# Kernel tuning notes

Hardware: AMD Instinct MI355X
Metric: run time of the kernel (lower is better)

The kernel has to match this reference:

```python
import jax, jax.numpy as jnp
import numpy as np

N_NODES = 100000
N_EDGES = 1200000
D = 64
EPS = 1e-12  # matches torch F.normalize eps


def l2norm(x):
    n = jnp.linalg.norm(x, axis=-1, keepdims=True)
    return x / jnp.maximum(n, EPS)


def sage_layer(x, src, dst, Wl, bl, Wr, scale):
    # mechanism.normalize: row-wise L2 normalize (noise_scale=0 -> perturb is identity)
    xn = l2norm(x)
    # agg = x_normalized + scatter-add of neighbor (source) features into targets
    agg = xn + jax.ops.segment_sum(xn[src], dst, num_segments=N_NODES)
    # MessageNorm(learn_scale=True): normalize(msg) * ||x||_2 * scale
    msg = l2norm(agg) * jnp.linalg.norm(x, axis=-1, keepdims=True) * scale
    # lin_l(msg) + lin_r(x)  (root_weight=True, lin_r has no bias)
    out = msg @ Wl.T + bl + x @ Wr.T
    return l2norm(out)


def setup_inputs() -> dict:
    key = jax.random.key(0)
    ks = jax.random.split(key, 7)
    s = 1.0 / np.sqrt(D)
    return {
        "x": jax.random.normal(ks[0], (N_NODES, D), jnp.float32),
        "Wl0": jax.random.normal(ks[1], (D, D), jnp.float32) * s,
        "bl0": jnp.zeros((D,), jnp.float32),
        "Wr0": jax.random.normal(ks[2], (D, D), jnp.float32) * s,
        "scale0": jnp.ones((), jnp.float32),
        "Wl1": jax.random.normal(ks[3], (D, D), jnp.float32) * s,
        "bl1": jnp.zeros((D,), jnp.float32),
        "Wr1": jax.random.normal(ks[4], (D, D), jnp.float32) * s,
        "scale1": jnp.ones((), jnp.float32),
        "edge_index": jax.random.randint(ks[5], (2, N_EDGES), 0, N_NODES, dtype=jnp.int32),
    }


def reference(x, Wl0, bl0, Wr0, scale0, Wl1, bl1, Wr1, scale1, edge_index):
    src, dst = edge_index[0], edge_index[1]
    h = sage_layer(x, src, dst, Wl0, bl0, Wr0, scale0)
    h = jax.nn.relu(h)  # activation after layer 0 (not pred layer); dropout=identity (eval)
    h = sage_layer(h, src, dst, Wl1, bl1, Wr1, scale1)
    return h  # last layer of pred module: no bn/dropout/activation
```

## Files before the change

### kernel.cpp

```cpp
#include <hip/hip_runtime.h>

#define D 64
#define EPS 1e-12f
#define WPITCH 68
#define BSHIFT 8
#define BW 256
#define NBMAX 2048
#define NBLK 256

typedef unsigned short u16;

__device__ __forceinline__ float bf2f(u16 u) {
    return __uint_as_float(((unsigned)u) << 16);
}
__device__ __forceinline__ u16 f2bf(float f) {
    unsigned u = __float_as_uint(f);
    u += 0x7fffu + ((u >> 16) & 1u);
    return (u16)(u >> 16);
}
__device__ __forceinline__ float loadf(const void* p, size_t i, int bf) {
    return bf ? bf2f(((const u16*)p)[i]) : ((const float*)p)[i];
}
__device__ __forceinline__ float4 cvt4(ushort4 u) {
    return make_float4(bf2f(u.x), bf2f(u.y), bf2f(u.z), bf2f(u.w));
}

#define FMA4(acc, s, v)                       \
    do {                                      \
        acc.x = fmaf((s), (v).x, acc.x);      \
        acc.y = fmaf((s), (v).y, acc.y);      \
        acc.z = fmaf((s), (v).z, acc.z);      \
        acc.w = fmaf((s), (v).w, acc.w);      \
    } while (0)

__global__ __launch_bounds__(64) void detect_kernel(const u16* __restrict__ x,
                                                    int* __restrict__ flag) {
    int lane = threadIdx.x;
    int bad = 0;
    for (int i = 0; i < 64; ++i) {
        u16 u = x[lane * 64 + i];
        int e = (u >> 7) & 0xFF;
        if (e >= 0xC0) bad = 1;
    }
    unsigned long long b = __ballot(bad);
    if (lane == 0) *flag = (b == 0ull) ? 1 : 0;
}


__global__ __launch_bounds__(256) void zero_kernel(int* __restrict__ a, int n) {
    int i = blockIdx.x * blockDim.x + threadIdx.x;
    if (i < n) a[i] = 0;
}

__global__ __launch_bounds__(256) void bhist_kernel(const int* __restrict__ dst,
                                                    int* __restrict__ blockhist,
                                                    int E, int NB) {
    __shared__ int lh[NBMAX];
    const int b = blockIdx.x, t = threadIdx.x;
    const int per = (E + NBLK - 1) / NBLK;
    const int e0 = b * per, e1 = min(E, e0 + per);
    if (NB <= NBMAX) {
        for (int i = t; i < NB; i += 256) lh[i] = 0;
        __syncthreads();
        for (int e = e0 + t; e < e1; e += 256)
            atomicAdd(&lh[dst[e] >> BSHIFT], 1);
        __syncthreads();
        for (int i = t; i < NB; i += 256) blockhist[i * NBLK + b] = lh[i];
    } else {
        for (int e = e0 + t; e < e1; e += 256)
            atomicAdd(&blockhist[(dst[e] >> BSHIFT) * NBLK + b], 1);
    }
}

__global__ __launch_bounds__(256) void scanA_kernel(const int* __restrict__ a,
                                                    int* __restrict__ partials, int M) {
    int b = blockIdx.x, t = threadIdx.x;
    int base = b * 1024 + t * 4;
    int s = 0;
#pragma unroll
    for (int i = 0; i < 4; ++i) {
        int idx = base + i;
        if (idx < M) s += a[idx];
    }
    s += __shfl_xor(s, 32); s += __shfl_xor(s, 16); s += __shfl_xor(s, 8);
    s += __shfl_xor(s, 4);  s += __shfl_xor(s, 2);  s += __shfl_xor(s, 1);
    __shared__ int wt[4];
    if ((t & 63) == 0) wt[t >> 6] = s;
    __syncthreads();
    if (t == 0) partials[b] = wt[0] + wt[1] + wt[2] + wt[3];
}

__global__ __launch_bounds__(64) void scanB_kernel(int* __restrict__ partials, int NP) {
    int l = threadIdx.x;
    int total = 0;
    for (int base = 0; base < NP; base += 64) {
        int v = (base + l < NP) ? partials[base + l] : 0;
        int inc = v;
        for (int d = 1; d < 64; d <<= 1) {
            int u = __shfl_up(inc, d);
            if (l >= d) inc += u;
        }
        if (base + l < NP) partials[base + l] = inc - v + total;
        total += __shfl(inc, 63);
    }
}

__global__ __launch_bounds__(256) void scanC_kernel(const int* __restrict__ a,
                                                    const int* __restrict__ partials,
                                                    int* __restrict__ pos, int M) {
    int b = blockIdx.x, t = threadIdx.x;
    int base = b * 1024 + t * 4;
    int v[4];
    int s = 0;
#pragma unroll
    for (int i = 0; i < 4; ++i) {
        int idx = base + i;
        v[i] = (idx < M) ? a[idx] : 0;
        s += v[i];
    }
    int li = t & 63, w = t >> 6;
    int inc = s;
    for (int d = 1; d < 64; d <<= 1) {
        int u = __shfl_up(inc, d);
        if (li >= d) inc += u;
    }
    __shared__ int wt[4];
    if (li == 63) wt[w] = inc;
    __syncthreads();
    int woff = 0;
    for (int i = 0; i < w; ++i) woff += wt[i];
    int run = partials[b] + woff + (inc - s);
#pragma unroll
    for (int i = 0; i < 4; ++i) {
        int idx = base + i;
        if (idx < M) { pos[idx] = run; run += v[i]; }
    }
}

__global__ __launch_bounds__(256) void bmeta_kernel(const int* __restrict__ pos,
                                                    int* __restrict__ bcounts,
                                                    int* __restrict__ boffsets,
                                                    int NB, int E) {
    int i = blockIdx.x * blockDim.x + threadIdx.x;
    if (i < NB) {
        int s = pos[(size_t)i * NBLK];
        boffsets[i] = s;
        int nxt = (i + 1 < NB) ? pos[(size_t)(i + 1) * NBLK] : E;
        bcounts[i] = nxt - s;
    }
}

__global__ __launch_bounds__(256) void bfill_kernel(const int* __restrict__ src,
                                                    const int* __restrict__ dst,
                                                    int* __restrict__ pos,
                                                    int* __restrict__ bucket,
                                                    int E, int NB) {
    __shared__ int cur[NBMAX];
    const int b = blockIdx.x, t = threadIdx.x;
    const int per = (E + NBLK - 1) / NBLK;
    const int e0 = b * per, e1 = min(E, e0 + per);
    if (NB <= NBMAX) {
        for (int i = t; i < NB; i += 256) cur[i] = pos[(size_t)i * NBLK + b];
        __syncthreads();
        for (int e = e0 + t; e < e1; e += 256) {
            int s = src[e], d = dst[e];
            int p = atomicAdd(&cur[d >> BSHIFT], 1);
            bucket[p] = (s << BSHIFT) | (d & (BW - 1));
        }
    } else {
        for (int e = e0 + t; e < e1; e += 256) {
            int s = src[e], d = dst[e];
            int p = atomicAdd(&pos[(size_t)(d >> BSHIFT) * NBLK + b], 1);
            bucket[p] = (s << BSHIFT) | (d & (BW - 1));
        }
    }
}

__global__ __launch_bounds__(256) void csr_from_buckets_kernel(
    const int* __restrict__ bucket,
    const int* __restrict__ bcounts, const int* __restrict__ boffsets,
    int* __restrict__ counts, int* __restrict__ offsets,
    int* __restrict__ sorted_src, int N)
{
    __shared__ int hist[BW];
    __shared__ int cur[BW];
    __shared__ int wt[4];

    const int b = blockIdx.x;
    const int t = threadIdx.x;
    const int nbase = b << BSHIFT;
    const int ecnt = bcounts[b];
    const int ebase = boffsets[b];

    hist[t] = 0;
    __syncthreads();

    for (int e = t; e < ecnt; e += 256)
        atomicAdd(&hist[bucket[ebase + e] & (BW - 1)], 1);
    __syncthreads();

    int v = hist[t];
    int inc = v;
    for (int d = 1; d < 64; d <<= 1) {
        int u = __shfl_up(inc, d);
        if ((t & 63) >= d) inc += u;
    }
    if ((t & 63) == 63) wt[t >> 6] = inc;
    __syncthreads();
    int woff = 0;
    for (int i = 0; i < (t >> 6); ++i) woff += wt[i];
    int excl = inc - v + woff;
    cur[t] = excl;
    int node = nbase + t;
    if (node < N) {
        counts[node] = v;
        offsets[node] = ebase + excl;
    }
    __syncthreads();

    for (int e = t; e < ecnt; e += 256) {
        int pv = bucket[ebase + e];
        int p = atomicAdd(&cur[pv & (BW - 1)], 1);
        sorted_src[ebase + p] = ((unsigned)pv) >> BSHIFT;
    }
}


__global__ __launch_bounds__(256) void norm_init_kernel(
    const void* __restrict__ xin, float* __restrict__ nx, float* __restrict__ rnx,
    int N, const int* __restrict__ flagp)
{
    const int bf = *flagp;
    int node = (int)((blockIdx.x * blockDim.x + threadIdx.x) >> 6);
    int lane = threadIdx.x & 63;
    if (node >= N) return;
    float v = loadf(xin, (size_t)node * D + lane, bf);
    float s = v * v;
    s += __shfl_xor(s, 32); s += __shfl_xor(s, 16); s += __shfl_xor(s, 8);
    s += __shfl_xor(s, 4);  s += __shfl_xor(s, 2);  s += __shfl_xor(s, 1);
    if (lane == 0) {
        float n = sqrtf(s);
        nx[node] = n;
        rnx[node] = 1.0f / fmaxf(n, EPS);
    }
}

__device__ __forceinline__ float4 loadrow4(const void* p, int row, int lane16, int bf) {
    if (bf) {
        ushort4 u = ((const ushort4*)((const u16*)p + (size_t)row * D))[lane16];
        return cvt4(u);
    }
    return ((const float4*)((const float*)p + (size_t)row * D))[lane16];
}

__global__ __launch_bounds__(256) void gather_kernel(
    const int* __restrict__ offsets, const int* __restrict__ counts,
    const int* __restrict__ sorted_src,
    const void* __restrict__ xin, const float* __restrict__ rnx,
    float* __restrict__ agg, int N, const int* __restrict__ flagp)
{
    const int bf = *flagp;
    int node = (int)((blockIdx.x * blockDim.x + threadIdx.x) >> 6);
    int lane = threadIdx.x & 63;
    if (node >= N) return;
    const int lane16 = lane & 15, grp = lane >> 4;

    float4 acc = make_float4(0.f, 0.f, 0.f, 0.f);
    if (grp == 0) {
        float4 xs = loadrow4(xin, node, lane16, bf);
        FMA4(acc, rnx[node], xs);
    }

    const int start = offsets[node];
    const int deg = counts[node];
    for (int i = 0; i < deg; i += 64) {
        int cnt = min(deg - i, 64);
        int id = (lane < cnt) ? sorted_src[start + i + lane] : 0;
        float wvl = rnx[id];
        int j = 0;
        for (; j + 8 <= cnt; j += 8) {
            int s0 = __shfl(id, j + grp);
            int s1 = __shfl(id, j + 4 + grp);
            float w0 = __shfl(wvl, j + grp);
            float w1 = __shfl(wvl, j + 4 + grp);
            float4 v0 = loadrow4(xin, s0, lane16, bf);
            float4 v1 = loadrow4(xin, s1, lane16, bf);
            FMA4(acc, w0, v0);
            FMA4(acc, w1, v1);
        }
        if (j + 4 <= cnt) {
            int s0 = __shfl(id, j + grp);
            float w0 = __shfl(wvl, j + grp);
            float4 v0 = loadrow4(xin, s0, lane16, bf);
            FMA4(acc, w0, v0);
            j += 4;
        }
        if (j < cnt) {
            int e = j + grp;
            int s0 = __shfl(id, min(e, cnt - 1));
            float w0 = __shfl(wvl, min(e, cnt - 1));
            if (e < cnt) {
                float4 v0 = loadrow4(xin, s0, lane16, bf);
                FMA4(acc, w0, v0);
            }
        }
    }

    acc.x += __shfl_xor(acc.x, 16); acc.y += __shfl_xor(acc.y, 16);
    acc.z += __shfl_xor(acc.z, 16); acc.w += __shfl_xor(acc.w, 16);
    acc.x += __shfl_xor(acc.x, 32); acc.y += __shfl_xor(acc.y, 32);
    acc.z += __shfl_xor(acc.z, 32); acc.w += __shfl_xor(acc.w, 32);
    if (grp == 0)
        ((float4*)(agg + (size_t)node * D))[lane16] = acc;
}

#define KSTEP(kk, comp)                                                     \
    {                                                                       \
        float4 a = *((const float4*)(wlp + (kk) * WPITCH));                 \
        float4 b = *((const float4*)(wrp + (kk) * WPITCH));                 \
        FMA4(acc[0], m[0].comp, a); FMA4(acc[0], xf[0].comp, b);            \
        FMA4(acc[1], m[1].comp, a); FMA4(acc[1], xf[1].comp, b);            \
        FMA4(acc[2], m[2].comp, a); FMA4(acc[2], xf[2].comp, b);            \
        FMA4(acc[3], m[3].comp, a); FMA4(acc[3], xf[3].comp, b);            \
    }

__global__ __launch_bounds__(256) void epilogue_kernel(
    const float* __restrict__ agg, float* __restrict__ nx,
    float* __restrict__ rnx, const void* __restrict__ xin,
    const void* __restrict__ wl, const void* __restrict__ bl,
    const void* __restrict__ wr, const void* __restrict__ scale_p,
    void* __restrict__ out, int N, const int* __restrict__ flagp,
    int relu, int write_norm)
{
    __shared__ float lds_wl[D * WPITCH];
    __shared__ float lds_wr[D * WPITCH];
    __shared__ float lds_bl[D];
    __shared__ float msgbuf[4][16 * WPITCH];

    const int bf = *flagp;
    const int t = threadIdx.x;
    for (int idx = t; idx < D * D; idx += 256) {
        int j = idx >> 6, k = idx & 63;
        lds_wl[k * WPITCH + j] = loadf(wl, idx, bf);
        lds_wr[k * WPITCH + j] = loadf(wr, idx, bf);
    }
    if (t < D) lds_bl[t] = loadf(bl, t, bf);
    __syncthreads();

    const float scl = loadf(scale_p, 0, bf);
    const int w = t >> 6, lane = t & 63;
    const int sub = lane >> 4, cg = lane & 15;
    float* mrow = msgbuf[w];

    for (int g = 0; g < 2; ++g) {
        const int node0 = blockIdx.x * 128 + g * 64 + w * 16 + sub * 4;
        int n[4];
        bool valid[4];
        float4 a4[4];
        float nxv[4];
#pragma unroll
        for (int r = 0; r < 4; ++r) {
            int nn = node0 + r;
            valid[r] = nn < N;
            n[r] = valid[r] ? nn : N - 1;
            a4[r] = ((const float4*)(agg + (size_t)n[r] * D))[cg];
            nxv[r] = nx[n[r]];
        }

#pragma unroll
        for (int r = 0; r < 4; ++r) {
            float4 v4 = a4[r];
            float s = v4.x * v4.x + v4.y * v4.y + v4.z * v4.z + v4.w * v4.w;
            s += __shfl_xor(s, 1); s += __shfl_xor(s, 2);
            s += __shfl_xor(s, 4); s += __shfl_xor(s, 8);
            float minv = scl * nxv[r] / fmaxf(sqrtf(s), EPS);
            *((float4*)(mrow + (sub * 4 + r) * WPITCH + cg * 4)) =
                make_float4(v4.x * minv, v4.y * minv, v4.z * minv, v4.w * minv);
        }

        float4 acc[4];
        {
            float4 b4 = ((const float4*)lds_bl)[cg];
#pragma unroll
            for (int r = 0; r < 4; ++r) acc[r] = b4;
        }

        const float* wlbase = lds_wl + cg * 4;
        const float* wrbase = lds_wr + cg * 4;

        if (bf) {
#pragma unroll
            for (int k4 = 0; k4 < 16; ++k4) {
                float4 m[4], xf[4];
#pragma unroll
                for (int r = 0; r < 4; ++r) {
                    m[r] = *((const float4*)(mrow + (sub * 4 + r) * WPITCH + k4 * 4));
                    ushort4 xu =
                        ((const ushort4*)((const u16*)xin + (size_t)n[r] * D))[k4];
                    xf[r] = cvt4(xu);
                }
                const float* wlp = wlbase + (k4 * 4) * WPITCH;
                const float* wrp = wrbase + (k4 * 4) * WPITCH;
                KSTEP(0, x) KSTEP(1, y) KSTEP(2, z) KSTEP(3, w)
            }
        } else {
#pragma unroll
            for (int k4 = 0; k4 < 16; ++k4) {
                float4 m[4], xf[4];
#pragma unroll
                for (int r = 0; r < 4; ++r) {
                    m[r] = *((const float4*)(mrow + (sub * 4 + r) * WPITCH + k4 * 4));
                    xf[r] = ((const float4*)((const float*)xin + (size_t)n[r] * D))[k4];
                }
                const float* wlp = wlbase + (k4 * 4) * WPITCH;
                const float* wrp = wrbase + (k4 * 4) * WPITCH;
                KSTEP(0, x) KSTEP(1, y) KSTEP(2, z) KSTEP(3, w)
            }
        }

#pragma unroll
        for (int r = 0; r < 4; ++r) {
            float4 v = acc[r];
            float s2 = v.x * v.x + v.y * v.y + v.z * v.z + v.w * v.w;
            s2 += __shfl_xor(s2, 1); s2 += __shfl_xor(s2, 2);
            s2 += __shfl_xor(s2, 4); s2 += __shfl_xor(s2, 8);
            float inv = 1.0f / fmaxf(sqrtf(s2), EPS);
            float4 rv = make_float4(v.x * inv, v.y * inv, v.z * inv, v.w * inv);
            if (relu) {
                rv.x = fmaxf(rv.x, 0.f); rv.y = fmaxf(rv.y, 0.f);
                rv.z = fmaxf(rv.z, 0.f); rv.w = fmaxf(rv.w, 0.f);
            }
            if (write_norm) {
                float s3 = rv.x * rv.x + rv.y * rv.y + rv.z * rv.z + rv.w * rv.w;
                s3 += __shfl_xor(s3, 1); s3 += __shfl_xor(s3, 2);
                s3 += __shfl_xor(s3, 4); s3 += __shfl_xor(s3, 8);
                if (valid[r] && cg == 0) {
                    float nn = sqrtf(s3);
                    nx[n[r]] = nn;
                    rnx[n[r]] = 1.0f / fmaxf(nn, EPS);
                }
            }
            if (valid[r]) {
                if (bf) {
                    ushort4 o =
                        make_ushort4(f2bf(rv.x), f2bf(rv.y), f2bf(rv.z), f2bf(rv.w));
                    ((ushort4*)((u16*)out + (size_t)n[r] * D))[cg] = o;
                } else {
                    ((float4*)((float*)out + (size_t)n[r] * D))[cg] = rv;
                }
            }
        }
    }
}

extern "C" void kernel_launch(void* const* d_in, const int* in_sizes, int n_in,
                              void* d_out, int out_size, void* d_ws, size_t ws_size,
                              hipStream_t stream)
{
    const void* x   = d_in[0];
    const void* Wl0 = d_in[1];
    const void* bl0 = d_in[2];
    const void* Wr0 = d_in[3];
    const void* sc0 = d_in[4];
    const void* Wl1 = d_in[5];
    const void* bl1 = d_in[6];
    const void* Wr1 = d_in[7];
    const void* sc1 = d_in[8];
    const int* ei   = (const int*)d_in[9];

    const int N = in_sizes[0] / D;
    const int E = in_sizes[9] / 2;
    const int* src = ei;
    const int* dst = ei + E;

    const int NB = (N + BW - 1) >> BSHIFT;
    const int M  = NB * NBLK;
    const int NP = (M + 1023) / 1024;

    float* agg       = (float*)d_ws;
    float* nx        = agg + (size_t)N * D;
    float* rnx       = nx + N;
    int* flag        = (int*)(rnx + N);
    int* counts      = flag + 1;
    int* offsets     = counts + N;
    int* bcounts     = offsets + N;
    int* boffsets    = bcounts + NB;
    int* blockhist   = boffsets + NB;
    int* pos         = blockhist + M;
    int* partials    = pos + M;
    int* bucket      = partials + NP;
    int* sorted_src  = bucket + E;

    void* h = d_out;

    dim3 blk(256);
    int gridA  = (N + 3) / 4;
    int gridC  = (N + 127) / 128;

    detect_kernel<<<1, 64, 0, stream>>>((const u16*)x, flag);

    if (NB > NBMAX)
        zero_kernel<<<(M + 255) / 256, blk, 0, stream>>>(blockhist, M);
    bhist_kernel<<<NBLK, blk, 0, stream>>>(dst, blockhist, E, NB);
    scanA_kernel<<<NP, blk, 0, stream>>>(blockhist, partials, M);
    scanB_kernel<<<1, 64, 0, stream>>>(partials, NP);
    scanC_kernel<<<NP, blk, 0, stream>>>(blockhist, partials, pos, M);
    bmeta_kernel<<<(NB + 255) / 256, blk, 0, stream>>>(pos, bcounts, boffsets, NB, E);
    bfill_kernel<<<NBLK, blk, 0, stream>>>(src, dst, pos, bucket, E, NB);
    csr_from_buckets_kernel<<<NB, blk, 0, stream>>>(bucket, bcounts, boffsets,
                                                    counts, offsets, sorted_src, N);

    norm_init_kernel<<<gridA, blk, 0, stream>>>(x, nx, rnx, N, flag);
    gather_kernel<<<gridA, blk, 0, stream>>>(offsets, counts, sorted_src, x, rnx,
                                             agg, N, flag);
    epilogue_kernel<<<gridC, blk, 0, stream>>>(agg, nx, rnx, x, Wl0, bl0, Wr0, sc0,
                                               h, N, flag, 1, 1);

    gather_kernel<<<gridA, blk, 0, stream>>>(offsets, counts, sorted_src, h, rnx,
                                             agg, N, flag);
    epilogue_kernel<<<gridC, blk, 0, stream>>>(agg, nx, rnx, h, Wl1, bl1, Wr1, sc1,
                                               d_out, N, flag, 0, 0);
}
```

Measured before the change: 401.0 us.

## Fold scan-B and bucket-meta kernels into neighbors, halve epilogue nodes per block

Removes the single-block scanB kernel by having each scanC block sum the preceding partials itself, and removes bmeta_kernel by computing bucket offsets and counts directly from pos inside csr_from_buckets. The epilogue kernel now handles 64 nodes per block instead of looping over two groups of 64, doubling the grid. This cuts two kernel launches and a serial stage, at the cost of redundant partial-sum reads in scanC and a reload of the LDS weights in twice as many blocks.

```diff
diff --git a/kernel.cpp b/kernel.cpp
--- a/kernel.cpp
+++ b/kernel.cpp
@@ -90,25 +90,23 @@
     if (t == 0) partials[b] = wt[0] + wt[1] + wt[2] + wt[3];
 }
 
-__global__ __launch_bounds__(64) void scanB_kernel(int* __restrict__ partials, int NP) {
-    int l = threadIdx.x;
-    int total = 0;
-    for (int base = 0; base < NP; base += 64) {
-        int v = (base + l < NP) ? partials[base + l] : 0;
-        int inc = v;
-        for (int d = 1; d < 64; d <<= 1) {
-            int u = __shfl_up(inc, d);
-            if (l >= d) inc += u;
-        }
-        if (base + l < NP) partials[base + l] = inc - v + total;
-        total += __shfl(inc, 63);
-    }
-}
-
 __global__ __launch_bounds__(256) void scanC_kernel(const int* __restrict__ a,
                                                     const int* __restrict__ partials,
-                                                    int* __restrict__ pos, int M) {
-    int b = blockIdx.x, t = threadIdx.x;
+                                                    int* __restrict__ pos,
+                                                    int M, int NP) {
+    const int b = blockIdx.x, t = threadIdx.x;
+    __shared__ int bwt[4];
+    __shared__ int wt[4];
+
+    int mysum = 0;
+    for (int i = t; i < b; i += 256) mysum += partials[i];
+    mysum += __shfl_xor(mysum, 32); mysum += __shfl_xor(mysum, 16);
+    mysum += __shfl_xor(mysum, 8);  mysum += __shfl_xor(mysum, 4);
+    mysum += __shfl_xor(mysum, 2);  mysum += __shfl_xor(mysum, 1);
+    if ((t & 63) == 0) bwt[t >> 6] = mysum;
+    __syncthreads();
+    const int base_sum = bwt[0] + bwt[1] + bwt[2] + bwt[3];
+
     int base = b * 1024 + t * 4;
     int v[4];
     int s = 0;
@@ -124,29 +122,15 @@
         int u = __shfl_up(inc, d);
         if (li >= d) inc += u;
     }
-    __shared__ int wt[4];
     if (li == 63) wt[w] = inc;
     __syncthreads();
     int woff = 0;
     for (int i = 0; i < w; ++i) woff += wt[i];
-    int run = partials[b] + woff + (inc - s);
+    int run = base_sum + woff + (inc - s);
 #pragma unroll
     for (int i = 0; i < 4; ++i) {
         int idx = base + i;
         if (idx < M) { pos[idx] = run; run += v[i]; }
-    }
-}
-
-__global__ __launch_bounds__(256) void bmeta_kernel(const int* __restrict__ pos,
-                                                    int* __restrict__ bcounts,
-                                                    int* __restrict__ boffsets,
-                                                    int NB, int E) {
-    int i = blockIdx.x * blockDim.x + threadIdx.x;
-    if (i < NB) {
-        int s = pos[(size_t)i * NBLK];
-        boffsets[i] = s;
-        int nxt = (i + 1 < NB) ? pos[(size_t)(i + 1) * NBLK] : E;
-        bcounts[i] = nxt - s;
     }
 }
 
@@ -177,10 +161,9 @@
 }
 
 __global__ __launch_bounds__(256) void csr_from_buckets_kernel(
-    const int* __restrict__ bucket,
-    const int* __restrict__ bcounts, const int* __restrict__ boffsets,
+    const int* __restrict__ bucket, const int* __restrict__ pos,
     int* __restrict__ counts, int* __restrict__ offsets,
-    int* __restrict__ sorted_src, int N)
+    int* __restrict__ sorted_src, int N, int E, int NB)
 {
     __shared__ int hist[BW];
     __shared__ int cur[BW];
@@ -189,8 +172,9 @@
     const int b = blockIdx.x;
     const int t = threadIdx.x;
     const int nbase = b << BSHIFT;
-    const int ecnt = bcounts[b];
-    const int ebase = boffsets[b];
+    const int ebase = pos[(size_t)b * NBLK];
+    const int enext = (b + 1 < NB) ? pos[(size_t)(b + 1) * NBLK] : E;
+    const int ecnt = enext - ebase;
 
     hist[t] = 0;
     __syncthreads();
@@ -350,104 +334,100 @@
     const float scl = loadf(scale_p, 0, bf);
     const int w = t >> 6, lane = t & 63;
     const int sub = lane >> 4, cg = lane & 15;
-    float* mrow = msgbuf[w];
-
-    for (int g = 0; g < 2; ++g) {
-        const int node0 = blockIdx.x * 128 + g * 64 + w * 16 + sub * 4;
-        int n[4];
-        bool valid[4];
-        float4 a4[4];
-        float nxv[4];
-#pragma unroll
-        for (int r = 0; r < 4; ++r) {
-            int nn = node0 + r;
-            valid[r] = nn < N;
-            n[r] = valid[r] ? nn : N - 1;
-            a4[r] = ((const float4*)(agg + (size_t)n[r] * D))[cg];
-            nxv[r] = nx[n[r]];
-        }
-
-#pragma unroll
-        for (int r = 0; r < 4; ++r) {
-            float4 v4 = a4[r];
-            float s = v4.x * v4.x + v4.y * v4.y + v4.z * v4.z + v4.w * v4.w;
-            s += __shfl_xor(s, 1); s += __shfl_xor(s, 2);
-            s += __shfl_xor(s, 4); s += __shfl_xor(s, 8);
-            float minv = scl * nxv[r] / fmaxf(sqrtf(s), EPS);
-            *((float4*)(mrow + (sub * 4 + r) * WPITCH + cg * 4)) =
-                make_float4(v4.x * minv, v4.y * minv, v4.z * minv, v4.w * minv);
-        }
-
-        float4 acc[4];
-        {
-            float4 b4 = ((const float4*)lds_bl)[cg];
-#pragma unroll
-            for (int r = 0; r < 4; ++r) acc[r] = b4;
-        }
-
-        const float* wlbase = lds_wl + cg * 4;
-        const float* wrbase = lds_wr + cg * 4;
-
-        if (bf) {
-#pragma unroll
-            for (int k4 = 0; k4 < 16; ++k4) {
-                float4 m[4], xf[4];
-#pragma unroll
-                for (int r = 0; r < 4; ++r) {
-                    m[r] = *((const float4*)(mrow + (sub * 4 + r) * WPITCH + k4 * 4));
-                    ushort4 xu =
-                        ((const ushort4*)((const u16*)xin + (size_t)n[r] * D))[k4];
-                    xf[r] = cvt4(xu);
-                }
-                const float* wlp = wlbase + (k4 * 4) * WPITCH;
-                const float* wrp = wrbase + (k4 * 4) * WPITCH;
-                KSTEP(0, x) KSTEP(1, y) KSTEP(2, z) KSTEP(3, w)
+
+    const int node0 = blockIdx.x * 64 + w * 16 + sub * 4;
+    int n[4];
+    bool valid[4];
+    float4 a4[4];
+    float nxv[4];
+#pragma unroll
+    for (int r = 0; r < 4; ++r) {
+        int nn = node0 + r;
+        valid[r] = nn < N;
+        n[r] = valid[r] ? nn : N - 1;
+        a4[r] = ((const float4*)(agg + (size_t)n[r] * D))[cg];
+        nxv[r] = nx[n[r]];
+    }
+
+    float* mrow = &msgbuf[w][sub * 4 * WPITCH];
+#pragma unroll
+    for (int r = 0; r < 4; ++r) {
+        float4 v4 = a4[r];
+        float s = v4.x * v4.x + v4.y * v4.y + v4.z * v4.z + v4.w * v4.w;
+        s += __shfl_xor(s, 1); s += __shfl_xor(s, 2);
+        s += __shfl_xor(s, 4); s += __shfl_xor(s, 8);
+        float minv = scl * nxv[r] / fmaxf(sqrtf(s), EPS);
+        *((float4*)(mrow + r * WPITCH + cg * 4)) =
+            make_float4(v4.x * minv, v4.y * minv, v4.z * minv, v4.w * minv);
+    }
+
+    float4 acc[4];
+    {
+        float4 b4 = ((const float4*)lds_bl)[cg];
+#pragma unroll
+        for (int r = 0; r < 4; ++r) acc[r] = b4;
+    }
+
+    const float* wlbase = lds_wl + cg * 4;
+    const float* wrbase = lds_wr + cg * 4;
+
+    if (bf) {
+#pragma unroll
+        for (int k4 = 0; k4 < 16; ++k4) {
+            float4 m[4], xf[4];
+#pragma unroll
+            for (int r = 0; r < 4; ++r) {
+                m[r] = *((const float4*)(mrow + r * WPITCH + k4 * 4));
+                ushort4 xu = ((const ushort4*)((const u16*)xin + (size_t)n[r] * D))[k4];
+                xf[r] = cvt4(xu);
             }
-        } else {
-#pragma unroll
-            for (int k4 = 0; k4 < 16; ++k4) {
-                float4 m[4], xf[4];
-#pragma unroll
-                for (int r = 0; r < 4; ++r) {
-                    m[r] = *((const float4*)(mrow + (sub * 4 + r) * WPITCH + k4 * 4));
-                    xf[r] = ((const float4*)((const float*)xin + (size_t)n[r] * D))[k4];
-                }
-                const float* wlp = wlbase + (k4 * 4) * WPITCH;
-                const float* wrp = wrbase + (k4 * 4) * WPITCH;
-                KSTEP(0, x) KSTEP(1, y) KSTEP(2, z) KSTEP(3, w)
+            const float* wlp = wlbase + (k4 * 4) * WPITCH;
+            const float* wrp = wrbase + (k4 * 4) * WPITCH;
+            KSTEP(0, x) KSTEP(1, y) KSTEP(2, z) KSTEP(3, w)
+        }
+    } else {
+#pragma unroll
+        for (int k4 = 0; k4 < 16; ++k4) {
+            float4 m[4], xf[4];
+#pragma unroll
+            for (int r = 0; r < 4; ++r) {
+                m[r] = *((const float4*)(mrow + r * WPITCH + k4 * 4));
+                xf[r] = ((const float4*)((const float*)xin + (size_t)n[r] * D))[k4];
             }
-        }
-
-#pragma unroll
-        for (int r = 0; r < 4; ++r) {
-            float4 v = acc[r];
-            float s2 = v.x * v.x + v.y * v.y + v.z * v.z + v.w * v.w;
-            s2 += __shfl_xor(s2, 1); s2 += __shfl_xor(s2, 2);
-            s2 += __shfl_xor(s2, 4); s2 += __shfl_xor(s2, 8);
-            float inv = 1.0f / fmaxf(sqrtf(s2), EPS);
-            float4 rv = make_float4(v.x * inv, v.y * inv, v.z * inv, v.w * inv);
-            if (relu) {
-                rv.x = fmaxf(rv.x, 0.f); rv.y = fmaxf(rv.y, 0.f);
-                rv.z = fmaxf(rv.z, 0.f); rv.w = fmaxf(rv.w, 0.f);
+            const float* wlp = wlbase + (k4 * 4) * WPITCH;
+            const float* wrp = wrbase + (k4 * 4) * WPITCH;
+            KSTEP(0, x) KSTEP(1, y) KSTEP(2, z) KSTEP(3, w)
+        }
+    }
+
+#pragma unroll
+    for (int r = 0; r < 4; ++r) {
+        float4 v = acc[r];
+        float s2 = v.x * v.x + v.y * v.y + v.z * v.z + v.w * v.w;
+        s2 += __shfl_xor(s2, 1); s2 += __shfl_xor(s2, 2);
+        s2 += __shfl_xor(s2, 4); s2 += __shfl_xor(s2, 8);
+        float inv = 1.0f / fmaxf(sqrtf(s2), EPS);
+        float4 rv = make_float4(v.x * inv, v.y * inv, v.z * inv, v.w * inv);
+        if (relu) {
+            rv.x = fmaxf(rv.x, 0.f); rv.y = fmaxf(rv.y, 0.f);
+            rv.z = fmaxf(rv.z, 0.f); rv.w = fmaxf(rv.w, 0.f);
+        }
+        if (write_norm) {
+            float s3 = rv.x * rv.x + rv.y * rv.y + rv.z * rv.z + rv.w * rv.w;
+            s3 += __shfl_xor(s3, 1); s3 += __shfl_xor(s3, 2);
+            s3 += __shfl_xor(s3, 4); s3 += __shfl_xor(s3, 8);
+            if (valid[r] && cg == 0) {
+                float nn = sqrtf(s3);
+                nx[n[r]] = nn;
+                rnx[n[r]] = 1.0f / fmaxf(nn, EPS);
             }
-            if (write_norm) {
-                float s3 = rv.x * rv.x + rv.y * rv.y + rv.z * rv.z + rv.w * rv.w;
-                s3 += __shfl_xor(s3, 1); s3 += __shfl_xor(s3, 2);
-                s3 += __shfl_xor(s3, 4); s3 += __shfl_xor(s3, 8);
-                if (valid[r] && cg == 0) {
-                    float nn = sqrtf(s3);
-                    nx[n[r]] = nn;
-                    rnx[n[r]] = 1.0f / fmaxf(nn, EPS);
-                }
-            }
-            if (valid[r]) {
-                if (bf) {
-                    ushort4 o =
-                        make_ushort4(f2bf(rv.x), f2bf(rv.y), f2bf(rv.z), f2bf(rv.w));
-                    ((ushort4*)((u16*)out + (size_t)n[r] * D))[cg] = o;
-                } else {
-                    ((float4*)((float*)out + (size_t)n[r] * D))[cg] = rv;
-                }
+        }
+        if (valid[r]) {
+            if (bf) {
+                ushort4 o = make_ushort4(f2bf(rv.x), f2bf(rv.y), f2bf(rv.z), f2bf(rv.w));
+                ((ushort4*)((u16*)out + (size_t)n[r] * D))[cg] = o;
+            } else {
+                ((float4*)((float*)out + (size_t)n[r] * D))[cg] = rv;
             }
         }
     }
@@ -483,9 +463,7 @@
     int* flag        = (int*)(rnx + N);
     int* counts      = flag + 1;
     int* offsets     = counts + N;
-    int* bcounts     = offsets + N;
-    int* boffsets    = bcounts + NB;
-    int* blockhist   = boffsets + NB;
+    int* blockhist   = offsets + N;
     int* pos         = blockhist + M;
     int* partials    = pos + M;
     int* bucket      = partials + NP;
@@ -495,7 +473,7 @@
 
     dim3 blk(256);
     int gridA  = (N + 3) / 4;
-    int gridC  = (N + 127) / 128;
+    int gridC  = (N + 63) / 64;
 
     detect_kernel<<<1, 64, 0, stream>>>((const u16*)x, flag);
 
@@ -503,12 +481,10 @@
         zero_kernel<<<(M + 255) / 256, blk, 0, stream>>>(blockhist, M);
     bhist_kernel<<<NBLK, blk, 0, stream>>>(dst, blockhist, E, NB);
     scanA_kernel<<<NP, blk, 0, stream>>>(blockhist, partials, M);
-    scanB_kernel<<<1, 64, 0, stream>>>(partials, NP);
-    scanC_kernel<<<NP, blk, 0, stream>>>(blockhist, partials, pos, M);
-    bmeta_kernel<<<(NB + 255) / 256, blk, 0, stream>>>(pos, bcounts, boffsets, NB, E);
+    scanC_kernel<<<NP, blk, 0, stream>>>(blockhist, partials, pos, M, NP);
     bfill_kernel<<<NBLK, blk, 0, stream>>>(src, dst, pos, bucket, E, NB);
-    csr_from_buckets_kernel<<<NB, blk, 0, stream>>>(bucket, bcounts, boffsets,
-                                                    counts, offsets, sorted_src, N);
+    csr_from_buckets_kernel<<<NB, blk, 0, stream>>>(bucket, pos, counts, offsets,
+                                                    sorted_src, N, E, NB);
 
     norm_init_kernel<<<gridA, blk, 0, stream>>>(x, nx, rnx, N, flag);
     gather_kernel<<<gridA, blk, 0, stream>>>(offsets, counts, sorted_src, x, rnx,
```

Result: slower. 416.4 us (+3.9%).
